# Kernel optimization log

Measured on AMD Instinct MI355X. Metric: run time of the kernel, lower is better.

The kernel has to match this reference:

```python
import jax, jax.numpy as jnp
import numpy as np

EPS = 1e-12  # matches torch F.normalize default eps
TEMPERATURE = 0.07

def _l2_normalize(x):
    norm = jnp.sqrt(jnp.sum(x * x, axis=-1, keepdims=True))
    return x / jnp.maximum(norm, EPS)

def setup_inputs() -> dict:
    key = jax.random.key(0)
    k1, k2 = jax.random.split(key)
    N, D = 4096, 1024
    z1 = jax.random.normal(k1, (N, D), dtype=jnp.float32)
    z2 = jax.random.normal(k2, (N, D), dtype=jnp.float32)
    return {"z1": z1, "z2": z2}

def reference(z1, z2):
    # L2-normalize both sets; cosine similarity of unit vectors is a dot product,
    # so the broadcast CosineSimilarity collapses to a single GEMM.
    z1n = _l2_normalize(z1)
    z2n = _l2_normalize(z2)
    logits = jnp.einsum('nd,md->nm', z1n, z2n) / TEMPERATURE  # [N, N]
    # CrossEntropyLoss with labels = arange(N): mean of -log_softmax diagonal.
    logp = jax.nn.log_softmax(logits, axis=-1)
    loss = -jnp.mean(jnp.diagonal(logp))
    return loss
```

## Files before the change

### kernel.cpp

```cpp
#include <hip/hip_runtime.h>

#define N_ROWS 4096
#define DIM 1024
#define INV_T (1.0f / 0.07f)
#define FP8_SCALE 16.0f
#define EXP_SCALE (INV_T * 1.44269504088896f / 256.0f)
#define BK 128
#define NJT 32

typedef __attribute__((ext_vector_type(4))) float floatx4;
typedef __attribute__((ext_vector_type(4))) int int4x;
typedef __attribute__((ext_vector_type(8))) int int8x;

#if __has_builtin(__builtin_amdgcn_cvt_pk_fp8_f32)
__device__ inline unsigned int pack4_e4m3(float x, float y, float z, float w) {
    int p = __builtin_amdgcn_cvt_pk_fp8_f32(x, y, 0, false);
    p = __builtin_amdgcn_cvt_pk_fp8_f32(z, w, p, true);
    return (unsigned int)p;
}
#else
__device__ inline unsigned int f2e4m3(float x) {
    unsigned int u = __float_as_uint(x);
    unsigned int s = (u >> 24) & 0x80u;
    int e = (int)((u >> 23) & 0xffu);
    unsigned int m = u & 0x7fffffu;
    if (e < 121) return s;
    unsigned int t = m >> 20;
    unsigned int rest = m & 0xFFFFFu;
    t += (rest > 0x80000u) || (rest == 0x80000u && (t & 1u));
    int e8 = e - 120;
    if (t == 8u) { t = 0u; e8 += 1; }
    return s | ((unsigned int)e8 << 3) | t;
}
__device__ inline unsigned int pack4_e4m3(float x, float y, float z, float w) {
    return f2e4m3(x) | (f2e4m3(y) << 8) | (f2e4m3(z) << 16) | (f2e4m3(w) << 24);
}
#endif

__global__ __launch_bounds__(256) void k_normalize(
    const float* __restrict__ z1, const float* __restrict__ z2,
    unsigned char* __restrict__ z1f, unsigned char* __restrict__ z2f,
    float* __restrict__ diag, float* __restrict__ out) {
    const int lane = threadIdx.x & 63, wave = threadIdx.x >> 6;
    const int row = blockIdx.x * 4 + wave;

    if (blockIdx.x == 0 && threadIdx.x == 0) out[0] = 0.f;

    const float4* A = reinterpret_cast<const float4*>(z1 + (size_t)row * DIM);
    const float4* B = reinterpret_cast<const float4*>(z2 + (size_t)row * DIM);
    float4 a[4], b[4];
    #pragma unroll
    for (int rep = 0; rep < 4; ++rep) {
        a[rep] = A[lane + 64 * rep];
        b[rep] = B[lane + 64 * rep];
    }

    float s11 = 0.f, s22 = 0.f, s12 = 0.f;
    #pragma unroll
    for (int rep = 0; rep < 4; ++rep) {
        s11 += a[rep].x * a[rep].x + a[rep].y * a[rep].y
             + a[rep].z * a[rep].z + a[rep].w * a[rep].w;
        s22 += b[rep].x * b[rep].x + b[rep].y * b[rep].y
             + b[rep].z * b[rep].z + b[rep].w * b[rep].w;
        s12 += a[rep].x * b[rep].x + a[rep].y * b[rep].y
             + a[rep].z * b[rep].z + a[rep].w * b[rep].w;
    }
    #pragma unroll
    for (int m = 32; m >= 1; m >>= 1) {
        s11 += __shfl_xor(s11, m, 64);
        s22 += __shfl_xor(s22, m, 64);
        s12 += __shfl_xor(s12, m, 64);
    }

    const float n1 = fmaxf(sqrtf(s11), 1e-12f);
    const float n2 = fmaxf(sqrtf(s22), 1e-12f);
    if (lane == 0) diag[row] = s12 / (n1 * n2) * INV_T;
    const float i1 = FP8_SCALE / n1, i2 = FP8_SCALE / n2;

    unsigned int* O1 = reinterpret_cast<unsigned int*>(z1f + (size_t)row * DIM);
    unsigned int* O2 = reinterpret_cast<unsigned int*>(z2f + (size_t)row * DIM);
    #pragma unroll
    for (int rep = 0; rep < 4; ++rep) {
        O1[lane + 64 * rep] = pack4_e4m3(a[rep].x * i1, a[rep].y * i1,
                                         a[rep].z * i1, a[rep].w * i1);
        O2[lane + 64 * rep] = pack4_e4m3(b[rep].x * i2, b[rep].y * i2,
                                         b[rep].z * i2, b[rep].w * i2);
    }
}

__global__ __launch_bounds__(256) void k_gemm_sumexp(
    const unsigned char* __restrict__ z1f, const unsigned char* __restrict__ z2f,
    float* __restrict__ P) {
    __shared__ __attribute__((aligned(16))) unsigned char As[128 * BK];
    __shared__ __attribute__((aligned(16))) unsigned char Bs[128 * BK];

    const int iT = blockIdx.y, jT = blockIdx.x;
    const int lane = threadIdx.x & 63, wave = threadIdx.x >> 6;
    const int wm = wave >> 1, wn = wave & 1;
    const int ml = lane & 15, q = lane >> 4;
    const int i0 = iT * 128, j0 = jT * 128;

    const int srow = lane >> 3;
    const int sg = ((lane & 7) ^ (srow & 7)) * 16;

    const int rs = ml & 7;
    const int slotL = ((2 * q) ^ rs) * 16;
    const int slotH = ((2 * q + 1) ^ rs) * 16;

    floatx4 acc[4][4];
    #pragma unroll
    for (int mt = 0; mt < 4; ++mt)
        #pragma unroll
        for (int nt = 0; nt < 4; ++nt)
            acc[mt][nt] = (floatx4){0.f, 0.f, 0.f, 0.f};

    for (int k0 = 0; k0 < DIM; k0 += BK) {
        #pragma unroll
        for (int c = 0; c < 4; ++c) {
            const int issue = wave * 4 + c;
            const int row = issue * 8 + srow;
            const unsigned char* gA = z1f + (size_t)(i0 + row) * DIM + k0 + sg;
            const unsigned char* gB = z2f + (size_t)(j0 + row) * DIM + k0 + sg;
            __builtin_amdgcn_global_load_lds(
                (const __attribute__((address_space(1))) void*)gA,
                (__attribute__((address_space(3))) void*)(As + issue * 1024), 16, 0, 0);
            __builtin_amdgcn_global_load_lds(
                (const __attribute__((address_space(1))) void*)gB,
                (__attribute__((address_space(3))) void*)(Bs + issue * 1024), 16, 0, 0);
        }
        __syncthreads();

        int8x af[4], bf[4];
        #pragma unroll
        for (int t = 0; t < 4; ++t) {
            const unsigned char* rowA = As + (wm * 64 + t * 16 + ml) * BK;
            const unsigned char* rowB = Bs + (wn * 64 + t * 16 + ml) * BK;
            int4x aL = *reinterpret_cast<const int4x*>(rowA + slotL);
            int4x aH = *reinterpret_cast<const int4x*>(rowA + slotH);
            int4x bLo = *reinterpret_cast<const int4x*>(rowB + slotL);
            int4x bHi = *reinterpret_cast<const int4x*>(rowB + slotH);
            af[t] = __builtin_shufflevector(aL, aH, 0, 1, 2, 3, 4, 5, 6, 7);
            bf[t] = __builtin_shufflevector(bLo, bHi, 0, 1, 2, 3, 4, 5, 6, 7);
        }
        #pragma unroll
        for (int mt = 0; mt < 4; ++mt)
            #pragma unroll
            for (int nt = 0; nt < 4; ++nt)
                acc[mt][nt] = __builtin_amdgcn_mfma_scale_f32_16x16x128_f8f6f4(
                    af[mt], bf[nt], acc[mt][nt],
                    0 , 0 ,
                    0, 0x7F , 0, 0x7F );
        __syncthreads();
    }

    float vv[4][4];
    #pragma unroll
    for (int mt = 0; mt < 4; ++mt) {
        #pragma unroll
        for (int r = 0; r < 4; ++r) {
            float v = 0.f;
            #pragma unroll
            for (int nt = 0; nt < 4; ++nt)
                v += __builtin_amdgcn_exp2f(acc[mt][nt][r] * EXP_SCALE);
            v += __shfl_xor(v, 1, 64);
            v += __shfl_xor(v, 2, 64);
            v += __shfl_xor(v, 4, 64);
            v += __shfl_xor(v, 8, 64);
            vv[mt][r] = v;
        }
    }
    float* Pl = reinterpret_cast<float*>(As);
    if (wn == 1 && ml == 0) {
        #pragma unroll
        for (int mt = 0; mt < 4; ++mt)
            #pragma unroll
            for (int r = 0; r < 4; ++r)
                Pl[wm * 64 + mt * 16 + q * 4 + r] = vv[mt][r];
    }
    __syncthreads();
    if (wn == 0 && ml == 0) {
        #pragma unroll
        for (int mt = 0; mt < 4; ++mt)
            #pragma unroll
            for (int r = 0; r < 4; ++r) {
                const int ri = wm * 64 + mt * 16 + q * 4 + r;
                P[jT * N_ROWS + i0 + ri] = vv[mt][r] + Pl[ri];
            }
    }
}

__global__ __launch_bounds__(128) void k_finalize(
    const float* __restrict__ P, const float* __restrict__ diag,
    float* __restrict__ out) {
    const int t = threadIdx.x;
    const int i = blockIdx.x * 128 + t;
    float s = 0.f;
    #pragma unroll
    for (int jt = 0; jt < NJT; ++jt)
        s += P[jt * N_ROWS + i];
    float v = logf(s) - diag[i];
    #pragma unroll
    for (int m = 32; m >= 1; m >>= 1)
        v += __shfl_xor(v, m, 64);
    __shared__ float r[2];
    if ((t & 63) == 0) r[t >> 6] = v;
    __syncthreads();
    if (t == 0) atomicAdd(out, (r[0] + r[1]) * (1.0f / N_ROWS));
}

extern "C" void kernel_launch(void* const* d_in, const int* in_sizes, int n_in,
                              void* d_out, int out_size, void* d_ws, size_t ws_size,
                              hipStream_t stream) {
    const float* z1 = (const float*)d_in[0];
    const float* z2 = (const float*)d_in[1];

    char* ws = (char*)d_ws;
    unsigned char* z1f = (unsigned char*)ws;
    unsigned char* z2f = (unsigned char*)(ws + (size_t)N_ROWS * DIM);
    float* diag = (float*)(ws + (size_t)N_ROWS * DIM * 2);
    float* P = diag + N_ROWS;

    k_normalize<<<N_ROWS / 4, 256, 0, stream>>>(z1, z2, z1f, z2f, diag,
                                                (float*)d_out);
    k_gemm_sumexp<<<dim3(NJT, 32), 256, 0, stream>>>(z1f, z2f, P);
    k_finalize<<<32, 128, 0, stream>>>(P, diag, (float*)d_out);
}
```

Baseline: 102.9 us.

## Use 256x256 tiles with double-buffered LDS and phased prefetch in FP8 GEMM

Enlarges the GEMM block tile from 128x128 to 256x256 with 512 threads (8 waves in a 2x4 layout) and double-buffers A and B in LDS. Each K-step is split into eight phases that interleave async global-to-LDS prefetches of the next tiles with MFMA work, using s_setprio and manual vmcnt waits. This is meant to hide load latency and raise operand reuse. The epilogue reduction is reworked to combine four column-wave partials through LDS, and the number of column partials per row is halved. The kernel now uses about 128KB of LDS per block, so only one block fits per CU, and the grid shrinks to 256 blocks.

```diff
diff --git a/kernel.cpp b/kernel.cpp
--- a/kernel.cpp
+++ b/kernel.cpp
@@ -6,11 +6,13 @@
 #define FP8_SCALE 16.0f
 #define EXP_SCALE (INV_T * 1.44269504088896f / 256.0f)
 #define BK 128
-#define NJT 32
+#define NJT 16
 
 typedef __attribute__((ext_vector_type(4))) float floatx4;
 typedef __attribute__((ext_vector_type(4))) int int4x;
 typedef __attribute__((ext_vector_type(8))) int int8x;
+
+template <int V> struct ic { static constexpr int v = V; };
 
 #if __has_builtin(__builtin_amdgcn_cvt_pk_fp8_f32)
 __device__ inline unsigned int pack4_e4m3(float x, float y, float z, float w) {
@@ -88,104 +90,144 @@
     }
 }
 
-__global__ __launch_bounds__(256) void k_gemm_sumexp(
+__global__ __launch_bounds__(512, 2) void k_gemm_sumexp(
     const unsigned char* __restrict__ z1f, const unsigned char* __restrict__ z2f,
     float* __restrict__ P) {
-    __shared__ __attribute__((aligned(16))) unsigned char As[128 * BK];
-    __shared__ __attribute__((aligned(16))) unsigned char Bs[128 * BK];
+    __shared__ __attribute__((aligned(16))) unsigned char As[2][256 * BK];
+    __shared__ __attribute__((aligned(16))) unsigned char Bs[2][256 * BK];
 
     const int iT = blockIdx.y, jT = blockIdx.x;
-    const int lane = threadIdx.x & 63, wave = threadIdx.x >> 6;
-    const int wm = wave >> 1, wn = wave & 1;
+    const int tid = threadIdx.x;
+    const int lane = tid & 63, wave = tid >> 6;
+    const int wm = wave >> 2, wn = wave & 3;
     const int ml = lane & 15, q = lane >> 4;
-    const int i0 = iT * 128, j0 = jT * 128;
+    const int i0 = iT * 256, j0 = jT * 256;
 
     const int srow = lane >> 3;
-    const int sg = ((lane & 7) ^ (srow & 7)) * 16;
-
-    const int rs = ml & 7;
-    const int slotL = ((2 * q) ^ rs) * 16;
-    const int slotH = ((2 * q + 1) ^ rs) * 16;
-
-    floatx4 acc[4][4];
-    #pragma unroll
-    for (int mt = 0; mt < 4; ++mt)
-        #pragma unroll
-        for (int nt = 0; nt < 4; ++nt)
-            acc[mt][nt] = (floatx4){0.f, 0.f, 0.f, 0.f};
-
-    for (int k0 = 0; k0 < DIM; k0 += BK) {
-        #pragma unroll
-        for (int c = 0; c < 4; ++c) {
-            const int issue = wave * 4 + c;
-            const int row = issue * 8 + srow;
-            const unsigned char* gA = z1f + (size_t)(i0 + row) * DIM + k0 + sg;
-            const unsigned char* gB = z2f + (size_t)(j0 + row) * DIM + k0 + sg;
+    const int sg = ((lane & 7) ^ srow) * 16;
+
+    floatx4 acc[2][4][2][2];
+    #pragma unroll
+    for (int mh = 0; mh < 2; ++mh)
+        #pragma unroll
+        for (int t = 0; t < 4; ++t)
+            #pragma unroll
+            for (int nh = 0; nh < 2; ++nh)
+                #pragma unroll
+                for (int n = 0; n < 2; ++n)
+                    acc[mh][t][nh][n] = (floatx4){0.f, 0.f, 0.f, 0.f};
+
+    auto stA = [&](int rbase, int tile, int dbuf) {
+        #pragma unroll
+        for (int u = 0; u < 2; ++u) {
+            const int lrow = rbase + wave * 16 + u * 8;
+            const unsigned char* g =
+                z1f + (size_t)(i0 + lrow + srow) * DIM + tile * BK + sg;
             __builtin_amdgcn_global_load_lds(
-                (const __attribute__((address_space(1))) void*)gA,
-                (__attribute__((address_space(3))) void*)(As + issue * 1024), 16, 0, 0);
+                (const __attribute__((address_space(1))) void*)g,
+                (__attribute__((address_space(3))) void*)(&As[dbuf][lrow * BK]),
+                16, 0, 0);
+        }
+    };
+    auto stB = [&](int rbase, int tile, int dbuf) {
+        #pragma unroll
+        for (int u = 0; u < 2; ++u) {
+            const int lrow = rbase + wave * 16 + u * 8;
+            const unsigned char* g =
+                z2f + (size_t)(j0 + lrow + srow) * DIM + tile * BK + sg;
             __builtin_amdgcn_global_load_lds(
-                (const __attribute__((address_space(1))) void*)gB,
-                (__attribute__((address_space(3))) void*)(Bs + issue * 1024), 16, 0, 0);
+                (const __attribute__((address_space(1))) void*)g,
+                (__attribute__((address_space(3))) void*)(&Bs[dbuf][lrow * BK]),
+                16, 0, 0);
         }
-        __syncthreads();
-
-        int8x af[4], bf[4];
-        #pragma unroll
-        for (int t = 0; t < 4; ++t) {
-            const unsigned char* rowA = As + (wm * 64 + t * 16 + ml) * BK;
-            const unsigned char* rowB = Bs + (wn * 64 + t * 16 + ml) * BK;
-            int4x aL = *reinterpret_cast<const int4x*>(rowA + slotL);
-            int4x aH = *reinterpret_cast<const int4x*>(rowA + slotH);
-            int4x bLo = *reinterpret_cast<const int4x*>(rowB + slotL);
-            int4x bHi = *reinterpret_cast<const int4x*>(rowB + slotH);
-            af[t] = __builtin_shufflevector(aL, aH, 0, 1, 2, 3, 4, 5, 6, 7);
-            bf[t] = __builtin_shufflevector(bLo, bHi, 0, 1, 2, 3, 4, 5, 6, 7);
-        }
-        #pragma unroll
-        for (int mt = 0; mt < 4; ++mt)
+    };
+
+    auto ldfrag = [&](const unsigned char* base, int row) -> int8x {
+        const int rs = row & 7;
+        const unsigned char* rp = base + row * BK;
+        int4x lo = *reinterpret_cast<const int4x*>(rp + (((2 * q) ^ rs) * 16));
+        int4x hi = *reinterpret_cast<const int4x*>(rp + (((2 * q + 1) ^ rs) * 16));
+        return __builtin_shufflevector(lo, hi, 0, 1, 2, 3, 4, 5, 6, 7);
+    };
+
+    auto phase = [&](auto Bc, auto Mc, auto Nc, auto stage, auto gate) {
+        constexpr int BUF = decltype(Bc)::v;
+        constexpr int MH = decltype(Mc)::v;
+        constexpr int NH = decltype(Nc)::v;
+        int8x af[4], bf[2];
+        #pragma unroll
+        for (int t = 0; t < 4; ++t)
+            af[t] = ldfrag(&As[BUF][0], MH * 128 + wm * 64 + t * 16 + ml);
+        #pragma unroll
+        for (int n = 0; n < 2; ++n)
+            bf[n] = ldfrag(&Bs[BUF][0], NH * 128 + wn * 32 + n * 16 + ml);
+        stage();
+        __builtin_amdgcn_s_barrier();
+        asm volatile("s_waitcnt lgkmcnt(0)" ::: "memory");
+        __builtin_amdgcn_s_setprio(1);
+        #pragma unroll
+        for (int t = 0; t < 4; ++t)
             #pragma unroll
-            for (int nt = 0; nt < 4; ++nt)
-                acc[mt][nt] = __builtin_amdgcn_mfma_scale_f32_16x16x128_f8f6f4(
-                    af[mt], bf[nt], acc[mt][nt],
+            for (int n = 0; n < 2; ++n)
+                acc[MH][t][NH][n] = __builtin_amdgcn_mfma_scale_f32_16x16x128_f8f6f4(
+                    af[t], bf[n], acc[MH][t][NH][n],
                     0 , 0 ,
                     0, 0x7F , 0, 0x7F );
-        __syncthreads();
-    }
-
-    float vv[4][4];
-    #pragma unroll
-    for (int mt = 0; mt < 4; ++mt) {
-        #pragma unroll
-        for (int r = 0; r < 4; ++r) {
-            float v = 0.f;
-            #pragma unroll
-            for (int nt = 0; nt < 4; ++nt)
-                v += __builtin_amdgcn_exp2f(acc[mt][nt][r] * EXP_SCALE);
-            v += __shfl_xor(v, 1, 64);
-            v += __shfl_xor(v, 2, 64);
-            v += __shfl_xor(v, 4, 64);
-            v += __shfl_xor(v, 8, 64);
-            vv[mt][r] = v;
-        }
-    }
-    float* Pl = reinterpret_cast<float*>(As);
-    if (wn == 1 && ml == 0) {
-        #pragma unroll
-        for (int mt = 0; mt < 4; ++mt)
-            #pragma unroll
-            for (int r = 0; r < 4; ++r)
-                Pl[wm * 64 + mt * 16 + q * 4 + r] = vv[mt][r];
-    }
-    __syncthreads();
-    if (wn == 0 && ml == 0) {
-        #pragma unroll
-        for (int mt = 0; mt < 4; ++mt)
+        __builtin_amdgcn_s_setprio(0);
+        gate();
+        __builtin_amdgcn_s_barrier();
+    };
+
+    stA(0, 0, 0);   stB(0, 0, 0);
+    stA(128, 0, 0); stB(128, 0, 0);
+    stA(0, 1, 1);   stB(0, 1, 1);
+    asm volatile("s_waitcnt vmcnt(4)" ::: "memory");
+    __builtin_amdgcn_s_barrier();
+
+    #pragma unroll
+    for (int t = 0; t < 4; ++t) {
+        phase(ic<0>{}, ic<0>{}, ic<0>{}, [&] { stA(128, 2 * t + 1, 1); }, [&] {});
+        phase(ic<0>{}, ic<0>{}, ic<1>{}, [&] { stB(128, 2 * t + 1, 1); }, [&] {});
+        phase(ic<0>{}, ic<1>{}, ic<0>{}, [&] { if (t < 3) stA(0, 2 * t + 2, 0); }, [&] {});
+        phase(ic<0>{}, ic<1>{}, ic<1>{}, [&] { if (t < 3) stB(0, 2 * t + 2, 0); },
+              [&] {
+                  if (t < 3) asm volatile("s_waitcnt vmcnt(4)" ::: "memory");
+                  else       asm volatile("s_waitcnt vmcnt(0)" ::: "memory");
+              });
+        phase(ic<1>{}, ic<0>{}, ic<0>{}, [&] { if (t < 3) stA(128, 2 * t + 2, 0); }, [&] {});
+        phase(ic<1>{}, ic<0>{}, ic<1>{}, [&] { if (t < 3) stB(128, 2 * t + 2, 0); }, [&] {});
+        phase(ic<1>{}, ic<1>{}, ic<0>{}, [&] { if (t < 3) stA(0, 2 * t + 3, 1); }, [&] {});
+        phase(ic<1>{}, ic<1>{}, ic<1>{}, [&] { if (t < 3) stB(0, 2 * t + 3, 1); },
+              [&] {
+                  if (t < 3) asm volatile("s_waitcnt vmcnt(4)" ::: "memory");
+                  else       asm volatile("s_waitcnt vmcnt(0)" ::: "memory");
+              });
+    }
+
+    float* Pl = reinterpret_cast<float*>(&As[0][0]);
+    #pragma unroll
+    for (int mh = 0; mh < 2; ++mh)
+        #pragma unroll
+        for (int t = 0; t < 4; ++t)
             #pragma unroll
             for (int r = 0; r < 4; ++r) {
-                const int ri = wm * 64 + mt * 16 + q * 4 + r;
-                P[jT * N_ROWS + i0 + ri] = vv[mt][r] + Pl[ri];
+                float v = 0.f;
+                #pragma unroll
+                for (int nh = 0; nh < 2; ++nh)
+                    #pragma unroll
+                    for (int n = 0; n < 2; ++n)
+                        v += __builtin_amdgcn_exp2f(acc[mh][t][nh][n][r] * EXP_SCALE);
+                v += __shfl_xor(v, 1, 64);
+                v += __shfl_xor(v, 2, 64);
+                v += __shfl_xor(v, 4, 64);
+                v += __shfl_xor(v, 8, 64);
+                if (ml == 0)
+                    Pl[wn * 256 + mh * 128 + wm * 64 + t * 16 + q * 4 + r] = v;
             }
+    __syncthreads();
+    if (tid < 256) {
+        float s = Pl[tid] + Pl[256 + tid] + Pl[512 + tid] + Pl[768 + tid];
+        P[jT * N_ROWS + i0 + tid] = s;
     }
 }
 
@@ -222,6 +264,6 @@
 
     k_normalize<<<N_ROWS / 4, 256, 0, stream>>>(z1, z2, z1f, z2f, diag,
                                                 (float*)d_out);
-    k_gemm_sumexp<<<dim3(NJT, 32), 256, 0, stream>>>(z1f, z2f, P);
+    k_gemm_sumexp<<<dim3(NJT, 16), 512, 0, stream>>>(z1f, z2f, P);
     k_finalize<<<32, 128, 0, stream>>>(P, diag, (float*)d_out);
 }
```

Result: slower. 405.1 us (+293.6%).

## Double-buffer LDS tiles to overlap global loads with MFMA compute

Applied to the files above, without the earlier changes.

The K loop of the FP8 GEMM now uses two LDS buffers for A and B. The next K-tile is prefetched via global_load_lds while MFMAs run on the current tile, and there is only one barrier per iteration. This aims to hide global memory latency that was previously exposed before each compute phase. It doubles LDS use to 64KB per block, which may reduce occupancy, and it relies on the remaining barrier being enough to order the async LDS writes against reads.

```diff
diff --git a/kernel.cpp b/kernel.cpp
--- a/kernel.cpp
+++ b/kernel.cpp
@@ -91,8 +91,8 @@
 __global__ __launch_bounds__(256) void k_gemm_sumexp(
     const unsigned char* __restrict__ z1f, const unsigned char* __restrict__ z2f,
     float* __restrict__ P) {
-    __shared__ __attribute__((aligned(16))) unsigned char As[128 * BK];
-    __shared__ __attribute__((aligned(16))) unsigned char Bs[128 * BK];
+    __shared__ __attribute__((aligned(16))) unsigned char As[2][128 * BK];
+    __shared__ __attribute__((aligned(16))) unsigned char Bs[2][128 * BK];
 
     const int iT = blockIdx.y, jT = blockIdx.x;
     const int lane = threadIdx.x & 63, wave = threadIdx.x >> 6;
@@ -101,7 +101,7 @@
     const int i0 = iT * 128, j0 = jT * 128;
 
     const int srow = lane >> 3;
-    const int sg = ((lane & 7) ^ (srow & 7)) * 16;
+    const int sg = ((lane & 7) ^ srow) * 16;
 
     const int rs = ml & 7;
     const int slotL = ((2 * q) ^ rs) * 16;
@@ -114,27 +114,48 @@
         for (int nt = 0; nt < 4; ++nt)
             acc[mt][nt] = (floatx4){0.f, 0.f, 0.f, 0.f};
 
-    for (int k0 = 0; k0 < DIM; k0 += BK) {
-        #pragma unroll
-        for (int c = 0; c < 4; ++c) {
-            const int issue = wave * 4 + c;
-            const int row = issue * 8 + srow;
-            const unsigned char* gA = z1f + (size_t)(i0 + row) * DIM + k0 + sg;
-            const unsigned char* gB = z2f + (size_t)(j0 + row) * DIM + k0 + sg;
-            __builtin_amdgcn_global_load_lds(
-                (const __attribute__((address_space(1))) void*)gA,
-                (__attribute__((address_space(3))) void*)(As + issue * 1024), 16, 0, 0);
-            __builtin_amdgcn_global_load_lds(
-                (const __attribute__((address_space(1))) void*)gB,
-                (__attribute__((address_space(3))) void*)(Bs + issue * 1024), 16, 0, 0);
+    #pragma unroll
+    for (int c = 0; c < 4; ++c) {
+        const int issue = wave * 4 + c;
+        const int row = issue * 8 + srow;
+        const unsigned char* gA = z1f + (size_t)(i0 + row) * DIM + sg;
+        const unsigned char* gB = z2f + (size_t)(j0 + row) * DIM + sg;
+        __builtin_amdgcn_global_load_lds(
+            (const __attribute__((address_space(1))) void*)gA,
+            (__attribute__((address_space(3))) void*)(&As[0][issue * 1024]), 16, 0, 0);
+        __builtin_amdgcn_global_load_lds(
+            (const __attribute__((address_space(1))) void*)gB,
+            (__attribute__((address_space(3))) void*)(&Bs[0][issue * 1024]), 16, 0, 0);
+    }
+    __syncthreads();
+
+    #pragma unroll
+    for (int kt = 0; kt < 8; ++kt) {
+        const int cur = kt & 1;
+        if (kt < 7) {
+            const int k0n = (kt + 1) * BK;
+            #pragma unroll
+            for (int c = 0; c < 4; ++c) {
+                const int issue = wave * 4 + c;
+                const int row = issue * 8 + srow;
+                const unsigned char* gA = z1f + (size_t)(i0 + row) * DIM + k0n + sg;
+                const unsigned char* gB = z2f + (size_t)(j0 + row) * DIM + k0n + sg;
+                __builtin_amdgcn_global_load_lds(
+                    (const __attribute__((address_space(1))) void*)gA,
+                    (__attribute__((address_space(3))) void*)(&As[cur ^ 1][issue * 1024]),
+                    16, 0, 0);
+                __builtin_amdgcn_global_load_lds(
+                    (const __attribute__((address_space(1))) void*)gB,
+                    (__attribute__((address_space(3))) void*)(&Bs[cur ^ 1][issue * 1024]),
+                    16, 0, 0);
+            }
         }
-        __syncthreads();
 
         int8x af[4], bf[4];
         #pragma unroll
         for (int t = 0; t < 4; ++t) {
-            const unsigned char* rowA = As + (wm * 64 + t * 16 + ml) * BK;
-            const unsigned char* rowB = Bs + (wn * 64 + t * 16 + ml) * BK;
+            const unsigned char* rowA = &As[cur][0] + (wm * 64 + t * 16 + ml) * BK;
+            const unsigned char* rowB = &Bs[cur][0] + (wn * 64 + t * 16 + ml) * BK;
             int4x aL = *reinterpret_cast<const int4x*>(rowA + slotL);
             int4x aH = *reinterpret_cast<const int4x*>(rowA + slotH);
             int4x bLo = *reinterpret_cast<const int4x*>(rowB + slotL);
@@ -169,7 +190,7 @@
             vv[mt][r] = v;
         }
     }
-    float* Pl = reinterpret_cast<float*>(As);
+    float* Pl = reinterpret_cast<float*>(&As[0][0]);
     if (wn == 1 && ml == 0) {
         #pragma unroll
         for (int mt = 0; mt < 4; ++mt)
```

After: 99.23 us (median of 2 runs). 3.6% less time.

## Double-buffer LDS tiles and prefetch MFMA fragments in FP8 GEMM loop

Applied to the files above, without the earlier changes.

The GEMM main loop now uses two LDS buffers for each of A and B. The global-to-LDS copy of tile k+2 is issued before the MFMAs of tile k, and the register fragments for tile k+1 are read ahead. The per-iteration __syncthreads pairs are replaced by explicit waitcnt plus barrier, so memory latency overlaps with matrix math. The cost is twice the LDS (64 KB per block), which may lower the number of resident blocks, and more registers for the double-buffered fragments.

```diff
diff --git a/kernel.cpp b/kernel.cpp
--- a/kernel.cpp
+++ b/kernel.cpp
@@ -91,8 +91,8 @@
 __global__ __launch_bounds__(256) void k_gemm_sumexp(
     const unsigned char* __restrict__ z1f, const unsigned char* __restrict__ z2f,
     float* __restrict__ P) {
-    __shared__ __attribute__((aligned(16))) unsigned char As[128 * BK];
-    __shared__ __attribute__((aligned(16))) unsigned char Bs[128 * BK];
+    __shared__ __attribute__((aligned(16))) unsigned char As[2][128 * BK];
+    __shared__ __attribute__((aligned(16))) unsigned char Bs[2][128 * BK];
 
     const int iT = blockIdx.y, jT = blockIdx.x;
     const int lane = threadIdx.x & 63, wave = threadIdx.x >> 6;
@@ -101,7 +101,7 @@
     const int i0 = iT * 128, j0 = jT * 128;
 
     const int srow = lane >> 3;
-    const int sg = ((lane & 7) ^ (srow & 7)) * 16;
+    const int sg = ((lane & 7) ^ srow) * 16;
 
     const int rs = ml & 7;
     const int slotL = ((2 * q) ^ rs) * 16;
@@ -114,7 +114,8 @@
         for (int nt = 0; nt < 4; ++nt)
             acc[mt][nt] = (floatx4){0.f, 0.f, 0.f, 0.f};
 
-    for (int k0 = 0; k0 < DIM; k0 += BK) {
+    auto stage = [&](int tile, int db) {
+        const int k0 = tile * BK;
         #pragma unroll
         for (int c = 0; c < 4; ++c) {
             const int issue = wave * 4 + c;
@@ -123,34 +124,51 @@
             const unsigned char* gB = z2f + (size_t)(j0 + row) * DIM + k0 + sg;
             __builtin_amdgcn_global_load_lds(
                 (const __attribute__((address_space(1))) void*)gA,
-                (__attribute__((address_space(3))) void*)(As + issue * 1024), 16, 0, 0);
+                (__attribute__((address_space(3))) void*)(&As[db][issue * 1024]),
+                16, 0, 0);
             __builtin_amdgcn_global_load_lds(
                 (const __attribute__((address_space(1))) void*)gB,
-                (__attribute__((address_space(3))) void*)(Bs + issue * 1024), 16, 0, 0);
+                (__attribute__((address_space(3))) void*)(&Bs[db][issue * 1024]),
+                16, 0, 0);
         }
-        __syncthreads();
-
-        int8x af[4], bf[4];
+    };
+
+    int8x af[2][4], bf[2][4];
+    auto ldfrags = [&](int sl, int db) {
         #pragma unroll
         for (int t = 0; t < 4; ++t) {
-            const unsigned char* rowA = As + (wm * 64 + t * 16 + ml) * BK;
-            const unsigned char* rowB = Bs + (wn * 64 + t * 16 + ml) * BK;
+            const unsigned char* rowA = &As[db][0] + (wm * 64 + t * 16 + ml) * BK;
+            const unsigned char* rowB = &Bs[db][0] + (wn * 64 + t * 16 + ml) * BK;
             int4x aL = *reinterpret_cast<const int4x*>(rowA + slotL);
             int4x aH = *reinterpret_cast<const int4x*>(rowA + slotH);
             int4x bLo = *reinterpret_cast<const int4x*>(rowB + slotL);
             int4x bHi = *reinterpret_cast<const int4x*>(rowB + slotH);
-            af[t] = __builtin_shufflevector(aL, aH, 0, 1, 2, 3, 4, 5, 6, 7);
-            bf[t] = __builtin_shufflevector(bLo, bHi, 0, 1, 2, 3, 4, 5, 6, 7);
+            af[sl][t] = __builtin_shufflevector(aL, aH, 0, 1, 2, 3, 4, 5, 6, 7);
+            bf[sl][t] = __builtin_shufflevector(bLo, bHi, 0, 1, 2, 3, 4, 5, 6, 7);
         }
+    };
+
+    stage(0, 0);
+    asm volatile("s_waitcnt vmcnt(0)" ::: "memory");
+    __builtin_amdgcn_s_barrier();
+    ldfrags(0, 0);
+    stage(1, 1);
+
+    #pragma unroll
+    for (int kt = 0; kt < 8; ++kt) {
+        const int cur = kt & 1;
+        asm volatile("s_waitcnt vmcnt(0) lgkmcnt(0)" ::: "memory");
+        __builtin_amdgcn_s_barrier();
+        if (kt < 7) ldfrags(cur ^ 1, cur ^ 1);
+        if (kt < 6) stage(kt + 2, cur);
         #pragma unroll
         for (int mt = 0; mt < 4; ++mt)
             #pragma unroll
             for (int nt = 0; nt < 4; ++nt)
                 acc[mt][nt] = __builtin_amdgcn_mfma_scale_f32_16x16x128_f8f6f4(
-                    af[mt], bf[nt], acc[mt][nt],
+                    af[cur][mt], bf[cur][nt], acc[mt][nt],
                     0 , 0 ,
                     0, 0x7F , 0, 0x7F );
-        __syncthreads();
     }
 
     float vv[4][4];
@@ -169,7 +187,7 @@
             vv[mt][r] = v;
         }
     }
-    float* Pl = reinterpret_cast<float*>(As);
+    float* Pl = reinterpret_cast<float*>(&As[0][0]);
     if (wn == 1 && ml == 0) {
         #pragma unroll
         for (int mt = 0; mt < 4; ++mt)
```

New measurement: 101.4 us. No clear change (-1.5%).
